# Optimization experiments

Measured on AMD Instinct MI355X. Metric: run time of the kernel, lower is better.

Reference implementation:

```python
import jax, jax.numpy as jnp
import numpy as np

NUM_HEADS = 4
NUM_TOTAL = 100000
N_HEDGE = 32768
N_NODE = 65536
MAX_ARITY_PAD = 10
MAX_VINE = 16
EMBED_DIM = 256
HIDDEN_DIM = 1024
N_LAYERS = 2
K_HOP = 2
POS_VOCAB = 23  # 2*max_arity+3
BATCH_PRED = 256


def setup_inputs() -> dict:
    key = jax.random.key(0)
    ks = jax.random.split(key, 16)
    s = 0.02
    D, FF, L = EMBED_DIM, HIDDEN_DIM, N_LAYERS
    unity_embeddings = jax.random.normal(ks[0], (NUM_TOTAL, D), jnp.float32) * s
    cls_edge_emb = jax.random.normal(ks[1], (1, D), jnp.float32) * s
    pad_edge_emb = jax.random.normal(ks[2], (1, D), jnp.float32) * s
    pos_table = jax.random.normal(ks[3], (POS_VOCAB, D), jnp.float32) * s
    qkv_w = jax.random.normal(ks[4], (L, 3 * D, D), jnp.float32) * s
    qkv_b = jnp.zeros((L, 3 * D), jnp.float32)
    out_w = jax.random.normal(ks[5], (L, D, D), jnp.float32) * s
    out_b = jnp.zeros((L, D), jnp.float32)
    ln1_g = jnp.ones((L, D), jnp.float32); ln1_b = jnp.zeros((L, D), jnp.float32)
    ln2_g = jnp.ones((L, D), jnp.float32); ln2_b = jnp.zeros((L, D), jnp.float32)
    ff1_w = jax.random.normal(ks[6], (L, FF, D), jnp.float32) * s
    ff1_b = jnp.zeros((L, FF), jnp.float32)
    ff2_w = jax.random.normal(ks[7], (L, D, FF), jnp.float32) * s
    ff2_b = jnp.zeros((L, D), jnp.float32)
    # V2E dense batch: entity/rel ids per hyperedge (padded to MAX_ARITY_PAD)
    xid_dense = jax.random.randint(ks[8], (N_HEDGE, MAX_ARITY_PAD), 0, NUM_TOTAL)
    v_mask = jax.random.bernoulli(ks[9], 0.7, (N_HEDGE, MAX_ARITY_PAD)).at[:, 0].set(True)
    x_pos = jax.random.randint(ks[10], (N_HEDGE, MAX_ARITY_PAD), 0, POS_VOCAB - 2)
    x_pos = jnp.where(v_mask, x_pos, POS_VOCAB - 2)  # pad pos id = 2*max_arity+1
    x_pos_dense = jnp.concatenate([jnp.full((N_HEDGE, 1), POS_VOCAB - 1, x_pos.dtype), x_pos], axis=1)  # cls pos id
    # E2V dense batch: hyperedge ids per node; pad id = N_HEDGE, cls id = N_HEDGE+1 (prepended)
    h_mask_body = jax.random.bernoulli(ks[11], 0.6, (N_NODE, MAX_VINE)).at[:, 0].set(True)
    hid_body = jax.random.randint(ks[12], (N_NODE, MAX_VINE), 0, N_HEDGE)
    hid_body = jnp.where(h_mask_body, hid_body, N_HEDGE)
    hid_dense = jnp.concatenate([jnp.full((N_NODE, 1), N_HEDGE + 1, hid_body.dtype), hid_body], axis=1)
    h_mask = jnp.concatenate([jnp.ones((N_NODE, 1), bool), h_mask_body], axis=1)
    subg_ent_id = jax.random.choice(ks[13], NUM_TOTAL, (N_NODE,), replace=False)
    predict_edge_index = jax.random.randint(ks[14], (BATCH_PRED,), 0, N_HEDGE)
    return dict(unity_embeddings=unity_embeddings, cls_edge_emb=cls_edge_emb, pad_edge_emb=pad_edge_emb,
                pos_table=pos_table, qkv_w=qkv_w, qkv_b=qkv_b, out_w=out_w, out_b=out_b,
                ln1_g=ln1_g, ln1_b=ln1_b, ln2_g=ln2_g, ln2_b=ln2_b,
                ff1_w=ff1_w, ff1_b=ff1_b, ff2_w=ff2_w, ff2_b=ff2_b,
                xid_dense=xid_dense, v_mask=v_mask, x_pos_dense=x_pos_dense,
                hid_dense=hid_dense, h_mask=h_mask, subg_ent_id=subg_ent_id,
                predict_edge_index=predict_edge_index, K_hop=K_HOP)


def _ln(x, g, b):
    m = jnp.mean(x, -1, keepdims=True)
    v = jnp.mean((x - m) ** 2, -1, keepdims=True)
    return (x - m) * jax.lax.rsqrt(v + 1e-5) * g + b


def _layer(x, mask, wqkv, bqkv, wo, bo, g1, b1, g2, b2, w1, bb1, w2, bb2):
    # Post-norm torch TransformerEncoderLayer with relu, dropout=0
    B, S, D = x.shape
    H = NUM_HEADS; dh = D // H
    qkv = x @ wqkv.T + bqkv
    q, k, v = jnp.split(qkv, 3, axis=-1)
    heads = lambda t: t.reshape(B, S, H, dh).transpose(0, 2, 1, 3)
    q, k, v = heads(q), heads(k), heads(v)
    scores = jnp.einsum('bhqd,bhkd->bhqk', q, k) / float(np.sqrt(dh))
    scores = jnp.where(mask[:, None, None, :], scores, -1e9)  # key padding mask
    attn = jax.nn.softmax(scores, axis=-1)
    o = jnp.einsum('bhqk,bhkd->bhqd', attn, v).transpose(0, 2, 1, 3).reshape(B, S, D)
    x = _ln(x + o @ wo.T + bo, g1, b1)
    f = jax.nn.relu(x @ w1.T + bb1) @ w2.T + bb2
    return _ln(x + f, g2, b2)


def _encoder(x, mask, qkv_w, qkv_b, out_w, out_b, ln1_g, ln1_b, ln2_g, ln2_b, ff1_w, ff1_b, ff2_w, ff2_b):
    for l in range(qkv_w.shape[0]):
        x = _layer(x, mask, qkv_w[l], qkv_b[l], out_w[l], out_b[l], ln1_g[l], ln1_b[l],
                   ln2_g[l], ln2_b[l], ff1_w[l], ff1_b[l], ff2_w[l], ff2_b[l])
    return x


def reference(unity_embeddings, cls_edge_emb, pad_edge_emb, pos_table, qkv_w, qkv_b, out_w, out_b,
              ln1_g, ln1_b, ln2_g, ln2_b, ff1_w, ff1_b, ff2_w, ff2_b,
              xid_dense, v_mask, x_pos_dense, hid_dense, h_mask, subg_ent_id, predict_edge_index, K_hop):
    D = unity_embeddings.shape[1]
    enc = lambda x, m: _encoder(x, m, qkv_w, qkv_b, out_w, out_b, ln1_g, ln1_b, ln2_g, ln2_b,
                                ff1_w, ff1_b, ff2_w, ff2_b)
    nE = xid_dense.shape[0]
    v_mask_cls = jnp.concatenate([jnp.ones((nE, 1), bool), v_mask], axis=1)
    unity = unity_embeddings
    h_out = None
    for k in range(K_hop + 1):
        # V2E: gather entities per hyperedge, prepend zero CLS, add positions
        xe = unity[xid_dense]                                         # [nE, A, D]
        xe = jnp.concatenate([jnp.zeros((nE, 1, D), xe.dtype), xe], axis=1)
        xe = xe + pos_table[x_pos_dense]
        he = enc(xe, v_mask_cls)[:, 0, :]                             # hedge emb = CLS output
        h_out = he[predict_edge_index]
        if k < K_hop:
            # E2V: hedge table + pad(id=nE) + cls(id=nE+1), gather per node
            ext = jnp.concatenate([he, pad_edge_emb, cls_edge_emb], axis=0)
            ve = ext[hid_dense]                                       # [nN, M+1, D]
            se = enc(ve, h_mask)[:, 0, :]
            unity = unity.at[subg_ent_id].set(se)
    return h_out
```

## Files before the change

### kernel.cpp

```cpp
#include <hip/hip_runtime.h>
#include <stdint.h>

typedef long long i64;
typedef __attribute__((ext_vector_type(8))) short bf16x8;
typedef __attribute__((ext_vector_type(4))) float f32x4;

#define SV 11
#define SE 17
#define ARITY 10
#define NHEDGE 32768
#define NNODE 65536
#define NTOTAL 100000
#define EXTROWS 32896
#define NPRED 256
#define MPRED 2816
#define NN1 2560
#define MN1 43520

__device__ __forceinline__ float b2f(ushort u) {
  union { uint32_t i; float f; } v; v.i = (uint32_t)u << 16; return v.f;
}
__device__ __forceinline__ ushort f2b(float f) {
  union { float f; uint32_t i; } v; v.f = f;
  uint32_t u = v.i + 0x7fffu + ((v.i >> 16) & 1u);
// ... 303 lines not shown
#pragma unroll
    for (int kh = 0; kh < 2; kh++)
#pragma unroll
      for (int m = 0; m < 4; m++)
#pragma unroll
        for (int n = 0; n < 4; n++)
          acc[m][n] = __builtin_amdgcn_mfma_f32_16x16x32_bf16(bf[kh][n], af[kh][m], acc[m][n], 0, 0, 0);
  }

#pragma unroll
  for (int m = 0; m < 4; m++) {
    const int row = m0 + (wr << 6) + (m << 4) + (lane & 15);
#pragma unroll
    for (int n = 0; n < 4; n++) {
      const int col = n0 + (wc << 6) + (n << 4) + ((lane >> 4) << 2);
      float v0 = acc[m][n][0], v1 = acc[m][n][1], v2 = acc[m][n][2], v3 = acc[m][n][3];
      if (MODE > 0) {
        const f32x4 bv = *(const f32x4*)&bias[col];
        v0 += bv[0]; v1 += bv[1]; v2 += bv[2]; v3 += bv[3];
      }
      if (MODE == 2) {
        v0 = fmaxf(v0, 0.f); v1 = fmaxf(v1, 0.f);
        v2 = fmaxf(v2, 0.f); v3 = fmaxf(v3, 0.f);
      }
      uint2 o; o.x = pack2(v0, v1); o.y = pack2(v2, v3);
      *(uint2*)&C[(i64)row * N + col] = o;
    }
  }
}

template <int K>
__global__ __launch_bounds__(512) void gemm_ln_k(const ushort* __restrict__ A,
                                                 const ushort* __restrict__ W,
                                                 const float* __restrict__ bias,
                                                 const ushort* R, int rstride,
                                                 const float* __restrict__ g,
                                                 const float* __restrict__ b,
                                                 ushort* C, int cstride, int M,
                                                 const int* ssn, int nseq,
                                                 const int* rrp) {
  const int m0 = blockIdx.x << 7;
  if (ssn && m0 >= ssn[nseq] - ssn[0]) return;
  __shared__ ushort As[128 * 64];
  __shared__ ushort Ws[256 * 64];
  __shared__ float partS[128][4];
  __shared__ float partQ[128][4];
  const int tid = threadIdx.x;
  const int wave = tid >> 6, lane = tid & 63;
  const int wr = wave >> 2, wc = wave & 3;

  f32x4 acc[4][4];
#pragma unroll
  for (int m = 0; m < 4; m++)
#pragma unroll
    for (int n = 0; n < 4; n++) acc[m][n] = (f32x4){0.f, 0.f, 0.f, 0.f};

  int rowA[2], kgA[2];
#pragma unroll
  for (int i = 0; i < 2; i++) {
    const int u = wave * 128 + i * 64 + lane;
    rowA[i] = u >> 3; kgA[i] = (u & 7) ^ ((u >> 3) & 7);
  }
  int rowW[4], kgW[4];
#pragma unroll
  for (int i = 0; i < 4; i++) {
    const int u = wave * 256 + i * 64 + lane;
    rowW[i] = u >> 3; kgW[i] = (u & 7) ^ ((u >> 3) & 7);
  }

#pragma unroll
  for (int i = 0; i < 2; i++)
    gload_lds16(A + (i64)(m0 + rowA[i]) * K + (kgA[i] << 3),
                (char*)As + (wave * 128 + i * 64) * 16);
#pragma unroll
  for (int i = 0; i < 4; i++)
    gload_lds16(W + (i64)rowW[i] * K + (kgW[i] << 3),
                (char*)Ws + (wave * 256 + i * 64) * 16);

  for (int k0 = 0; k0 < K; k0 += 64) {
    __syncthreads();
    bf16x8 af[2][4], bf[2][4];
#pragma unroll
    for (int kh = 0; kh < 2; kh++) {
      const int kb = (kh << 2) + (lane >> 4);
#pragma unroll
      for (int m = 0; m < 4; m++) {
        const int row = (wr << 6) + (m << 4) + (lane & 15);
        af[kh][m] = *(const bf16x8*)&As[row * 64 + ((kb ^ (row & 7)) << 3)];
      }
#pragma unroll
      for (int n = 0; n < 4; n++) {
        const int row = (wc << 6) + (n << 4) + (lane & 15);
        bf[kh][n] = *(const bf16x8*)&Ws[row * 64 + ((kb ^ (row & 7)) << 3)];
      }
    }
    __syncthreads();
    if (k0 + 64 < K) {
#pragma unroll
      for (int i = 0; i < 2; i++)
        gload_lds16(A + (i64)(m0 + rowA[i]) * K + (k0 + 64) + (kgA[i] << 3),
                    (char*)As + (wave * 128 + i * 64) * 16);
#pragma unroll
      for (int i = 0; i < 4; i++)
        gload_lds16(W + (i64)rowW[i] * K + (k0 + 64) + (kgW[i] << 3),
                    (char*)Ws + (wave * 256 + i * 64) * 16);
    }
#pragma unroll
    for (int kh = 0; kh < 2; kh++)
#pragma unroll
      for (int m = 0; m < 4; m++)
#pragma unroll
        for (int n = 0; n < 4; n++)
          acc[m][n] = __builtin_amdgcn_mfma_f32_16x16x32_bf16(bf[kh][n], af[kh][m], acc[m][n], 0, 0, 0);
  }

#pragma unroll
  for (int m = 0; m < 4; m++) {
    const int tokl = (wr << 6) + (m << 4) + (lane & 15);
    const int row = m0 + tokl;
    const i64 rr = rrp ? (i64)(rrp[row] - rrp[0]) : (i64)row;
    float s = 0.f, q = 0.f;
#pragma unroll
    for (int n = 0; n < 4; n++) {
      const int col = (wc << 6) + (n << 4) + ((lane >> 4) << 2);
      const f32x4 bv = *(const f32x4*)&bias[col];
      const uint2 ru = *(const uint2*)&R[rr * rstride + col];
      float v0 = acc[m][n][0] + bv[0] + b2f((ushort)(ru.x & 0xffff));
      float v1 = acc[m][n][1] + bv[1] + b2f((ushort)(ru.x >> 16));
      float v2 = acc[m][n][2] + bv[2] + b2f((ushort)(ru.y & 0xffff));
      float v3 = acc[m][n][3] + bv[3] + b2f((ushort)(ru.y >> 16));
      acc[m][n][0] = v0; acc[m][n][1] = v1; acc[m][n][2] = v2; acc[m][n][3] = v3;
      s += v0 + v1 + v2 + v3;
      q += v0 * v0 + v1 * v1 + v2 * v2 + v3 * v3;
    }
    s += __shfl_xor(s, 16, 64); s += __shfl_xor(s, 32, 64);
    q += __shfl_xor(q, 16, 64); q += __shfl_xor(q, 32, 64);
    if (lane < 16) { partS[tokl][wc] = s; partQ[tokl][wc] = q; }
  }
  __syncthreads();
#pragma unroll
  for (int m = 0; m < 4; m++) {
    const int tokl = (wr << 6) + (m << 4) + (lane & 15);
    const i64 row = (i64)(m0 + tokl);
    const f32x4 s4 = *(const f32x4*)&partS[tokl][0];
    const f32x4 q4 = *(const f32x4*)&partQ[tokl][0];
    const float mean = (s4[0] + s4[1] + s4[2] + s4[3]) * (1.f / 256.f);
    const float var = (q4[0] + q4[1] + q4[2] + q4[3]) * (1.f / 256.f) - mean * mean;
    const float rs = rsqrtf(var + 1e-5f);
#pragma unroll
    for (int n = 0; n < 4; n++) {
      const int col = (wc << 6) + (n << 4) + ((lane >> 4) << 2);
      const f32x4 g4 = *(const f32x4*)&g[col];
      const f32x4 b4 = *(const f32x4*)&b[col];
      uint2 o;
      o.x = pack2((acc[m][n][0] - mean) * rs * g4[0] + b4[0],
                  (acc[m][n][1] - mean) * rs * g4[1] + b4[1]);
      o.y = pack2((acc[m][n][2] - mean) * rs * g4[2] + b4[2],
                  (acc[m][n][3] - mean) * rs * g4[3] + b4[3]);
      *(uint2*)&C[row * cstride + col] = o;
    }
  }
}

template <int S>
__global__ __launch_bounds__(16 * S) void attn1_k(const ushort* __restrict__ QKV,
                                                  const int* __restrict__ ss,
                                                  ushort* __restrict__ O) {
  __shared__ float KL[4][S][68];
  __shared__ float VL[4][S][68];
  const int tid = threadIdx.x;
  const int s0 = ss[0];
  const int base = ss[blockIdx.x] - s0;
  const int L = ss[blockIdx.x + 1] - ss[blockIdx.x];

  for (int u = tid; u < 128 * L; u += 16 * S) {
    const int d4 = u & 15, h = (u >> 4) & 3, mt = u >> 6;
    const int mat = (mt >= L), t = mat ? mt - L : mt;
    const ushort* gp = QKV + (i64)(base + t) * 768 + 256 + mat * 256 + h * 64 + d4 * 4;
    ushort4 raw = *(const ushort4*)gp;
    float* dst = (mat ? &VL[h][t][0] : &KL[h][t][0]) + d4 * 4;
    dst[0] = b2f(raw.x); dst[1] = b2f(raw.y); dst[2] = b2f(raw.z); dst[3] = b2f(raw.w);
  }
  __syncthreads();

  const int h = tid / (4 * S);
  const int r = tid - h * 4 * S;
  const int q = r >> 2, j = r & 3;
  if (q >= L) return;

  float qv[16];
  {
    const ushort* qp = QKV + (i64)(base + q) * 768 + h * 64 + j * 16;
    cvt8(*(const uint4*)qp, qv);
    cvt8(*(const uint4*)(qp + 8), qv + 8);
  }

  float w[S];
  float mx = -1e30f;
#pragma unroll
  for (int s = 0; s < S; s++) {
    float p = -1e30f;
    if (s < L) {
      const float* kr = &KL[h][s][j * 16];
      p = 0.f;
#pragma unroll
      for (int e = 0; e < 4; e++) {
        const float4 kv = *(const float4*)(kr + e * 4);
        p = fmaf(qv[e * 4 + 0], kv.x, p);
        p = fmaf(qv[e * 4 + 1], kv.y, p);
        p = fmaf(qv[e * 4 + 2], kv.z, p);
        p = fmaf(qv[e * 4 + 3], kv.w, p);
      }
      p += __shfl_xor(p, 1, 64);
      p += __shfl_xor(p, 2, 64);
      p *= 0.125f;
    }
    w[s] = p;
    mx = fmaxf(mx, p);
  }
  float sum = 0.f;
#pragma unroll
  for (int s = 0; s < S; s++) { w[s] = __expf(w[s] - mx); sum += w[s]; }
  const float inv = 1.f / sum;

  float o[16];
#pragma unroll
  for (int e = 0; e < 16; e++) o[e] = 0.f;
#pragma unroll
  for (int s = 0; s < S; s++) {
    if (s < L) {
      const float ws = w[s];
      const float* vr = &VL[h][s][j * 16];
#pragma unroll
      for (int e = 0; e < 4; e++) {
        const float4 vv = *(const float4*)(vr + e * 4);
        o[e * 4 + 0] = fmaf(ws, vv.x, o[e * 4 + 0]);
        o[e * 4 + 1] = fmaf(ws, vv.y, o[e * 4 + 1]);
        o[e * 4 + 2] = fmaf(ws, vv.z, o[e * 4 + 2]);
        o[e * 4 + 3] = fmaf(ws, vv.w, o[e * 4 + 3]);
      }
    }
  }
  uint4 st0, st1;
  st0.x = pack2(o[0] * inv, o[1] * inv);   st0.y = pack2(o[2] * inv, o[3] * inv);
  st0.z = pack2(o[4] * inv, o[5] * inv);   st0.w = pack2(o[6] * inv, o[7] * inv);
  st1.x = pack2(o[8] * inv, o[9] * inv);   st1.y = pack2(o[10] * inv, o[11] * inv);
  st1.z = pack2(o[12] * inv, o[13] * inv); st1.w = pack2(o[14] * inv, o[15] * inv);
  ushort* op = O + (i64)(base + q) * 256 + h * 64 + j * 16;
  *(uint4*)op = st0;
  *(uint4*)(op + 8) = st1;
}

template <int S>
__global__ __launch_bounds__(16 * S) void attn1g_k(const ushort* __restrict__ QKVE,
                                                   const int* __restrict__ gid,
                                                   const int* __restrict__ ss,
                                                   ushort* __restrict__ O) {
  __shared__ float KL[4][S][68];
  __shared__ float VL[4][S][68];
  __shared__ int ids[S];
  const int tid = threadIdx.x;
  const int s0 = ss[0];
  const int base = ss[blockIdx.x] - s0;
  const int L = ss[blockIdx.x + 1] - ss[blockIdx.x];

  if (tid < L) ids[tid] = gid[base + tid];
  __syncthreads();

  for (int u = tid; u < 128 * L; u += 16 * S) {
    const int d4 = u & 15, h = (u >> 4) & 3, mt = u >> 6;
    const int mat = (mt >= L), t = mat ? mt - L : mt;
    const ushort* gp = QKVE + (i64)ids[t] * 768 + 256 + mat * 256 + h * 64 + d4 * 4;
    ushort4 raw = *(const ushort4*)gp;
    float* dst = (mat ? &VL[h][t][0] : &KL[h][t][0]) + d4 * 4;
    dst[0] = b2f(raw.x); dst[1] = b2f(raw.y); dst[2] = b2f(raw.z); dst[3] = b2f(raw.w);
  }
  __syncthreads();

  const int h = tid / (4 * S);
  const int r = tid - h * 4 * S;
  const int q = r >> 2, j = r & 3;
  if (q >= L) return;

  float qv[16];
  {
    const ushort* qp = QKVE + (i64)ids[q] * 768 + h * 64 + j * 16;
    cvt8(*(const uint4*)qp, qv);
    cvt8(*(const uint4*)(qp + 8), qv + 8);
  }

  float w[S];
  float mx = -1e30f;
#pragma unroll
  for (int s = 0; s < S; s++) {
    float p = -1e30f;
    if (s < L) {
      const float* kr = &KL[h][s][j * 16];
      p = 0.f;
#pragma unroll
      for (int e = 0; e < 4; e++) {
        const float4 kv = *(const float4*)(kr + e * 4);
        p = fmaf(qv[e * 4 + 0], kv.x, p);
        p = fmaf(qv[e * 4 + 1], kv.y, p);
        p = fmaf(qv[e * 4 + 2], kv.z, p);
        p = fmaf(qv[e * 4 + 3], kv.w, p);
      }
// ... 224 lines not shown
  const int lane = threadIdx.x & 63;
  ushort4 v = *(const ushort4*)&predHe[(i64)i * 256 + lane * 4];
  float4 o; o.x = b2f(v.x); o.y = b2f(v.y); o.z = b2f(v.z); o.w = b2f(v.w);
  *(float4*)&out[(i64)i * 256 + lane * 4] = o;
}

extern "C" void kernel_launch(void* const* d_in, const int* in_sizes, int n_in,
                              void* d_out, int out_size, void* d_ws, size_t ws_size,
                              hipStream_t stream) {
  (void)in_sizes; (void)n_in; (void)out_size;
  const float* unity_in = (const float*)d_in[0];
  const float* cls_emb  = (const float*)d_in[1];
  const float* pad_emb  = (const float*)d_in[2];
  const float* pos_tab  = (const float*)d_in[3];
  const float* qkv_w    = (const float*)d_in[4];
  const float* qkv_b    = (const float*)d_in[5];
  const float* out_w    = (const float*)d_in[6];
  const float* out_b    = (const float*)d_in[7];
  const float* ln1_g    = (const float*)d_in[8];
  const float* ln1_b    = (const float*)d_in[9];
  const float* ln2_g    = (const float*)d_in[10];
  const float* ln2_b    = (const float*)d_in[11];
  const float* ff1_w    = (const float*)d_in[12];
  const float* ff1_b    = (const float*)d_in[13];
  const float* ff2_w    = (const float*)d_in[14];
  const float* ff2_b    = (const float*)d_in[15];
  const int* xid   = (const int*)d_in[16];
  const int* vmask = (const int*)d_in[17];
  const int* xpos  = (const int*)d_in[18];
  const int* hid   = (const int*)d_in[19];
  const int* hmask = (const int*)d_in[20];
  const int* subg  = (const int*)d_in[21];
  const int* pred  = (const int*)d_in[22];

  const i64 unity_b = (i64)NTOTAL * 256 * 4;
  const i64 ext_b   = (i64)EXTROWS * 256 * 2;
  const i64 qkvE_b  = (i64)EXTROWS * 768 * 2;
  const int nq = 2 * 768 * 256, no = 2 * 256 * 256,
            n1 = 2 * 1024 * 256, n2 = 2 * 256 * 1024;
  const i64 wts_b = (i64)(nq + no + n1 + n2) * 2;
  const i64 idx_b = 16 * 1024 * 1024;
  const i64 per_elem = (i64)SE * (512 + 2048 + 512 + 4);
  int CHUNK = 8192;
  while (CHUNK > 4096 &&
         unity_b + ext_b + qkvE_b + wts_b + idx_b + (i64)CHUNK * per_elem > (i64)ws_size)
    CHUNK >>= 1;
  const int NCH_H = NHEDGE / CHUNK;
  const int NCH_N = NNODE / CHUNK;

  char* w = (char*)d_ws;
  float*  unity = (float*)w;  w += unity_b;
  ushort* ext   = (ushort*)w; w += ext_b;
  ushort* qkvE  = (ushort*)w; w += qkvE_b;
  ushort* wq    = (ushort*)w; w += (i64)nq * 2;
  ushort* wo    = (ushort*)w; w += (i64)no * 2;
  ushort* w1    = (ushort*)w; w += (i64)n1 * 2;
  ushort* w2    = (ushort*)w; w += (i64)n2 * 2;
  ushort* X     = (ushort*)w; w += (i64)CHUNK * SE * 256 * 2;
  ushort* Y     = (ushort*)w; w += (i64)CHUNK * SE * 1024 * 2;
  ushort* O     = (ushort*)w; w += (i64)CHUNK * SE * 256 * 2;
  int* gid    = (int*)w; w += (i64)CHUNK * SE * 4;
  int* inv    = (int*)w; w += (i64)NTOTAL * 4;
  int* cntE   = (int*)w; w += (i64)NNODE * 4;
  int* cntV   = (int*)w; w += (i64)NHEDGE * 4;
  int* partV  = (int*)w; w += 256 * 4;
  int* partN  = (int*)w; w += 256 * 4;
  int* partA  = (int*)w; w += 256 * 4;
  int* partB  = (int*)w; w += 256 * 4;
  int* ssV    = (int*)w; w += (i64)(NHEDGE + 1) * 4;
  int* ssP    = (int*)w; w += 257 * 4;
  int* ssN    = (int*)w; w += (i64)(NN1 + 1) * 4;
  int* nodeL  = (int*)w; w += (i64)NN1 * 4;
  int* cntN   = (int*)w; w += (i64)NN1 * 4;
  int* tokV   = (int*)w; w += (i64)NHEDGE * SV * 4;
  int* tokP   = (int*)w; w += MPRED * 4;
  int* tokN   = (int*)w; w += (i64)MN1 * 4;
  int* gidN   = (int*)w; w += (i64)MN1 * 4;
  int* flagH  = (int*)w; w += (i64)NHEDGE * 4;
  int* flagE  = (int*)w; w += (i64)NTOTAL * 4;
  int* posH   = (int*)w; w += (i64)(NHEDGE + 1) * 4;
  int* posN   = (int*)w; w += (i64)(NNODE + 1) * 4;
  int* hedgeL = (int*)w; w += (i64)NHEDGE * 4;
  int* nodeL0 = (int*)w; w += (i64)NNODE * 4;
  int* cntB   = (int*)w; w += (i64)NHEDGE * 4;
  int* cntC   = (int*)w; w += (i64)NNODE * 4;
  int* cntD   = (int*)w; w += (i64)NNODE * 4;
  int* ssH    = (int*)w; w += (i64)(NHEDGE + 1) * 4;
  int* ssN0   = (int*)w; w += (i64)(NNODE + 1) * 4;
  int* tokH   = (int*)w; w += (i64)NHEDGE * SV * 4;
  int* tokN0  = (int*)w; w += (i64)NNODE * SE * 4;
  int* ssHseq = (int*)w; w += 16 * 4;
  int* ssNseq = (int*)w; w += 16 * 4;
  ushort* predHe = (ushort*)w; w += (i64)NPRED * 256 * 2;
  ushort* Ocls = O;
  ushort* Qcls = O + (i64)CHUNK * 256;
  ushort* X2   = O + (i64)2 * CHUNK * 256;
  ushort* X3   = O + (i64)3 * CHUNK * 256;

  f2b_cvt_k<<<512, 256, 0, stream>>>(qkv_w, wq, nq);
  f2b_cvt_k<<<512, 256, 0, stream>>>(out_w, wo, no);
  f2b_cvt_k<<<512, 256, 0, stream>>>(ff1_w, w1, n1);
  f2b_cvt_k<<<512, 256, 0, stream>>>(ff2_w, w2, n2);
  hipMemcpyAsync(unity, unity_in, unity_b, hipMemcpyDeviceToDevice, stream);
  ext_init_k<<<1, 256, 0, stream>>>(ext, pad_emb, cls_emb);

  cnt_k<<<NHEDGE / 256, 256, 0, stream>>>(vmask, ARITY, 1, cntV, NHEDGE);
  scan1_k<<<NHEDGE / 256, 256, 0, stream>>>(cntV, ssV, partV, NHEDGE);
  scan2_k<<<1, 256, 0, stream>>>(partV, NHEDGE / 256, ssV, NHEDGE);
  scan3_k<<<NHEDGE / 256, 256, 0, stream>>>(ssV, partV, vmask, ARITY, 1, tokV, NHEDGE);
  cnt_k<<<NNODE / 256, 256, 0, stream>>>(hmask, SE, 0, cntE, NNODE);
  predscan_k<<<1, 256, 0, stream>>>(pred, cntV, vmask, ssP, tokP);
  inv_init_k<<<(NTOTAL + 255) / 256, 256, 0, stream>>>(inv, NTOTAL);
  inv_fill_k<<<NNODE / 256, 256, 0, stream>>>(subg, inv, NNODE);
  prednode_k<<<NN1 / 256, 256, 0, stream>>>(pred, xid, vmask, inv, cntE, nodeL, cntN);
  scan1_k<<<NN1 / 256, 256, 0, stream>>>(cntN, ssN, partN, NN1);
  scan2_k<<<1, 256, 0, stream>>>(partN, NN1 / 256, ssN, NN1);
  scan3n_k<<<NN1 / 256, 256, 0, stream>>>(ssN, partN, hmask, nodeL, tokN);
  zero_k<<<NHEDGE / 256, 256, 0, stream>>>(flagH, NHEDGE);
  zero_k<<<(NTOTAL + 255) / 256, 256, 0, stream>>>(flagE, NTOTAL);
  flagH_k<<<(NN1 * SE + 255) / 256, 256, 0, stream>>>(nodeL, hmask, hid, flagH);
  flagE_k<<<NHEDGE * ARITY / 256, 256, 0, stream>>>(flagH, vmask, xid, flagE);
  flagN_k<<<NNODE / 256, 256, 0, stream>>>(flagE, subg, cntC);
  scan1_k<<<NHEDGE / 256, 256, 0, stream>>>(flagH, posH, partA, NHEDGE);
  scan2_k<<<1, 256, 0, stream>>>(partA, NHEDGE / 256, posH, NHEDGE);
  fill_list_k<<<NHEDGE / 256, 256, 0, stream>>>(flagH, posH, partA, hedgeL, NHEDGE);
  cnt_list_k<<<NHEDGE / 256, 256, 0, stream>>>(hedgeL, posH + NHEDGE, cntV, cntB, NHEDGE);
  scan1_k<<<NHEDGE / 256, 256, 0, stream>>>(cntB, ssH, partA, NHEDGE);
  scan2_k<<<1, 256, 0, stream>>>(partA, NHEDGE / 256, ssH, NHEDGE);
  tok_hedge_k<<<NHEDGE / 256, 256, 0, stream>>>(ssH, partA, posH + NHEDGE, hedgeL, vmask, tokH);
  scan1_k<<<NNODE / 256, 256, 0, stream>>>(cntC, posN, partB, NNODE);
  scan2_k<<<1, 256, 0, stream>>>(partB, NNODE / 256, posN, NNODE);
  fill_list_k<<<NNODE / 256, 256, 0, stream>>>(cntC, posN, partB, nodeL0, NNODE);
  cnt_list_k<<<NNODE / 256, 256, 0, stream>>>(nodeL0, posN + NNODE, cntE, cntD, NNODE);
  scan1_k<<<NNODE / 256, 256, 0, stream>>>(cntD, ssN0, partB, NNODE);
  scan2_k<<<1, 256, 0, stream>>>(partB, NNODE / 256, ssN0, NNODE);
  tok_node_k<<<NNODE / 256, 256, 0, stream>>>(ssN0, partB, posN + NNODE, nodeL0, hmask, tokN0);
  seqlim_k<<<1, 64, 0, stream>>>(posH + NHEDGE, CHUNK, NCH_H, ssHseq);
  seqlim_k<<<1, 64, 0, stream>>>(posN + NNODE, CHUNK, NCH_N, ssNseq);

  const i64 KVo = (i64)768 * 256 + (i64)256 * 256;
  const i64 Qo  = (i64)768 * 256;

  for (int c = 0; c < NCH_H; c++) {
    const int e0 = c * CHUNK;
    const int* ssc = ssV + e0;
    const int Mmax = CHUNK * SV;
    gather_v2e_k<<<Mmax / 4, 256, 0, stream>>>(unity, pos_tab, xid, xpos,
                                               tokV, ssc, CHUNK, X);
    gemm_bf16_k<256, 1><<<dim3(6, Mmax / 128), 256, 0, stream>>>(
        X, wq, qkv_b, Y, Mmax, 768, ssc, CHUNK, nullptr);
    attn1_k<SV><<<CHUNK, 16 * SV, 0, stream>>>(Y, ssc, O);
    gemm_ln_k<256><<<Mmax / 128, 512, 0, stream>>>(
        O, wo, out_b, X, 256, ln1_g, ln1_b, X, 256, Mmax, ssc, CHUNK, nullptr);
    gemm_bf16_k<256, 2><<<dim3(8, Mmax / 128), 256, 0, stream>>>(
        X, w1, ff1_b, Y, Mmax, 1024, ssc, CHUNK, nullptr);
    gemm_ln_k<1024><<<Mmax / 128, 512, 0, stream>>>(
        Y, w2, ff2_b, X, 256, ln2_g, ln2_b, X, 256, Mmax, ssc, CHUNK, nullptr);
    gemm_bf16_k<256, 1><<<dim3(4, Mmax / 128), 256, 0, stream>>>(
        X, wq + KVo, qkv_b + 768 + 256, Y, Mmax, 512, ssc, CHUNK, nullptr);
    gemm_bf16_k<256, 1><<<dim3(2, CHUNK / 128), 256, 0, stream>>>(
        X, wq + Qo, qkv_b + 768, Qcls, CHUNK, 256, nullptr, 0, ssc);
    attn_cls_k<SV><<<CHUNK / 16, 256, 0, stream>>>(Qcls, Y, ssc, Ocls);
    gemm_ln_k<256><<<CHUNK / 128, 512, 0, stream>>>(
        Ocls, wo + (i64)256 * 256, out_b + 256, X, 256,
        ln1_g + 256, ln1_b + 256, X2, 256, CHUNK, nullptr, 0, ssc);
    gemm_bf16_k<256, 2><<<dim3(8, CHUNK / 128), 256, 0, stream>>>(
        X2, w1 + (i64)1024 * 256, ff1_b + 1024, Y, CHUNK, 1024, nullptr, 0, nullptr);
    gemm_ln_k<1024><<<CHUNK / 128, 512, 0, stream>>>(
        Y, w2 + (i64)256 * 1024, ff2_b + 256, X2, 256,
        ln2_g + 256, ln2_b + 256, ext + (i64)e0 * 256, 256, CHUNK, nullptr, 0, nullptr);
  }
  gemm_bf16_k<256, 1><<<dim3(6, EXTROWS / 128), 256, 0, stream>>>(
      ext, wq, qkv_b, qkvE, EXTROWS, 768, nullptr, 0, nullptr);

  for (int c = 0; c < NCH_N; c++) {
    const int base = c * CHUNK;
    const int* ssc = ssN0 + base;
    const int* sqc = ssNseq + c;
    const int Mmax = CHUNK * SE;
    gather_e2vc_k<<<Mmax / 4, 256, 0, stream>>>(ext, hid, nodeL0, tokN0, ssc, CHUNK, X, gid);
    attn1g_k<SE><<<CHUNK, 16 * SE, 0, stream>>>(qkvE, gid, ssc, O);
    gemm_ln_k<256><<<Mmax / 128, 512, 0, stream>>>(
        O, wo, out_b, X, 256, ln1_g, ln1_b, X, 256, Mmax, ssc, CHUNK, nullptr);
    gemm_bf16_k<256, 2><<<dim3(8, Mmax / 128), 256, 0, stream>>>(
        X, w1, ff1_b, Y, Mmax, 1024, ssc, CHUNK, nullptr);
    gemm_ln_k<1024><<<Mmax / 128, 512, 0, stream>>>(
        Y, w2, ff2_b, X, 256, ln2_g, ln2_b, X, 256, Mmax, ssc, CHUNK, nullptr);
    gemm_bf16_k<256, 1><<<dim3(4, Mmax / 128), 256, 0, stream>>>(
        X, wq + KVo, qkv_b + 768 + 256, Y, Mmax, 512, ssc, CHUNK, nullptr);
    gemm_bf16_k<256, 1><<<dim3(2, CHUNK / 128), 256, 0, stream>>>(
        X, wq + Qo, qkv_b + 768, Qcls, CHUNK, 256, sqc, 1, ssc);
    attn_cls_k<SE><<<CHUNK / 16, 256, 0, stream>>>(Qcls, Y, ssc, Ocls);
    gemm_ln_k<256><<<CHUNK / 128, 512, 0, stream>>>(
        Ocls, wo + (i64)256 * 256, out_b + 256, X, 256,
        ln1_g + 256, ln1_b + 256, X2, 256, CHUNK, sqc, 1, ssc);
    gemm_bf16_k<256, 2><<<dim3(8, CHUNK / 128), 256, 0, stream>>>(
        X2, w1 + (i64)1024 * 256, ff1_b + 1024, Y, CHUNK, 1024, sqc, 1, nullptr);
    gemm_ln_k<1024><<<CHUNK / 128, 512, 0, stream>>>(
        Y, w2 + (i64)256 * 1024, ff2_b + 256, X2, 256,
        ln2_g + 256, ln2_b + 256, X3, 256, CHUNK, sqc, 1, nullptr);
    scatter_nc_k<<<CHUNK / 4, 256, 0, stream>>>(X3, subg, nodeL0, posN + NNODE,
                                                unity, base);
  }

  for (int c = 0; c < NCH_H; c++) {
    const int base = c * CHUNK;
    const int* ssc = ssH + base;
    const int* sqc = ssHseq + c;
    const int Mmax = CHUNK * SV;
    gather_v2eh_k<<<Mmax / 4, 256, 0, stream>>>(unity, pos_tab, xid, xpos,
                                                hedgeL, tokH, ssc, CHUNK, X);
    gemm_bf16_k<256, 1><<<dim3(6, Mmax / 128), 256, 0, stream>>>(
        X, wq, qkv_b, Y, Mmax, 768, ssc, CHUNK, nullptr);
    attn1_k<SV><<<CHUNK, 16 * SV, 0, stream>>>(Y, ssc, O);
    gemm_ln_k<256><<<Mmax / 128, 512, 0, stream>>>(
        O, wo, out_b, X, 256, ln1_g, ln1_b, X, 256, Mmax, ssc, CHUNK, nullptr);
    gemm_bf16_k<256, 2><<<dim3(8, Mmax / 128), 256, 0, stream>>>(
        X, w1, ff1_b, Y, Mmax, 1024, ssc, CHUNK, nullptr);
    gemm_ln_k<1024><<<Mmax / 128, 512, 0, stream>>>(
        Y, w2, ff2_b, X, 256, ln2_g, ln2_b, X, 256, Mmax, ssc, CHUNK, nullptr);
    gemm_bf16_k<256, 1><<<dim3(4, Mmax / 128), 256, 0, stream>>>(
        X, wq + KVo, qkv_b + 768 + 256, Y, Mmax, 512, ssc, CHUNK, nullptr);
    gemm_bf16_k<256, 1><<<dim3(2, CHUNK / 128), 256, 0, stream>>>(
        X, wq + Qo, qkv_b + 768, Qcls, CHUNK, 256, sqc, 1, ssc);
    attn_cls_k<SV><<<CHUNK / 16, 256, 0, stream>>>(Qcls, Y, ssc, Ocls);
    gemm_ln_k<256><<<CHUNK / 128, 512, 0, stream>>>(
        Ocls, wo + (i64)256 * 256, out_b + 256, X, 256,
        ln1_g + 256, ln1_b + 256, X2, 256, CHUNK, sqc, 1, ssc);
    gemm_bf16_k<256, 2><<<dim3(8, CHUNK / 128), 256, 0, stream>>>(
        X2, w1 + (i64)1024 * 256, ff1_b + 1024, Y, CHUNK, 1024, sqc, 1, nullptr);
    gemm_ln_k<1024><<<CHUNK / 128, 512, 0, stream>>>(
        Y, w2 + (i64)256 * 1024, ff2_b + 256, X2, 256,
        ln2_g + 256, ln2_b + 256, X3, 256, CHUNK, sqc, 1, nullptr);
    scatter_ext_k<<<CHUNK / 4, 256, 0, stream>>>(X3, hedgeL, posH + NHEDGE, ext, base);
  }
  gemm_bf16_k<256, 1><<<dim3(6, EXTROWS / 128), 256, 0, stream>>>(
      ext, wq, qkv_b, qkvE, EXTROWS, 768, nullptr, 0, nullptr);

  {
    gather_e2vc_k<<<MN1 / 4, 256, 0, stream>>>(ext, hid, nodeL, tokN, ssN, NN1, X, gidN);
    attn1g_k<SE><<<NN1, 16 * SE, 0, stream>>>(qkvE, gidN, ssN, O);
    gemm_ln_k<256><<<MN1 / 128, 512, 0, stream>>>(
        O, wo, out_b, X, 256, ln1_g, ln1_b, X, 256, MN1, ssN, NN1, nullptr);
    gemm_bf16_k<256, 2><<<dim3(8, MN1 / 128), 256, 0, stream>>>(
        X, w1, ff1_b, Y, MN1, 1024, ssN, NN1, nullptr);
    gemm_ln_k<1024><<<MN1 / 128, 512, 0, stream>>>(
        Y, w2, ff2_b, X, 256, ln2_g, ln2_b, X, 256, MN1, ssN, NN1, nullptr);
    gemm_bf16_k<256, 1><<<dim3(4, MN1 / 128), 256, 0, stream>>>(
        X, wq + KVo, qkv_b + 768 + 256, Y, MN1, 512, ssN, NN1, nullptr);
    gemm_bf16_k<256, 1><<<dim3(2, NN1 / 128), 256, 0, stream>>>(
        X, wq + Qo, qkv_b + 768, Qcls, NN1, 256, nullptr, 0, ssN);
    attn_cls_k<SE><<<NN1 / 16, 256, 0, stream>>>(Qcls, Y, ssN, Ocls);
    gemm_ln_k<256><<<NN1 / 128, 512, 0, stream>>>(
        Ocls, wo + (i64)256 * 256, out_b + 256, X, 256,
        ln1_g + 256, ln1_b + 256, X2, 256, NN1, nullptr, 0, ssN);
    gemm_bf16_k<256, 2><<<dim3(8, NN1 / 128), 256, 0, stream>>>(
        X2, w1 + (i64)1024 * 256, ff1_b + 1024, Y, NN1, 1024, nullptr, 0, nullptr);
    gemm_ln_k<1024><<<NN1 / 128, 512, 0, stream>>>(
        Y, w2 + (i64)256 * 1024, ff2_b + 256, X2, 256,
        ln2_g + 256, ln2_b + 256, X3, 256, NN1, nullptr, 0, nullptr);
    scatter_nc_k<<<NN1 / 4, 256, 0, stream>>>(X3, subg, nodeL, nullptr, unity, 0);
  }

  {
    const int* ssc = ssP;
    gather_v2e_k<<<MPRED / 4, 256, 0, stream>>>(unity, pos_tab, xid, xpos,
                                                tokP, ssc, NPRED, X);
    gemm_bf16_k<256, 1><<<dim3(6, MPRED / 128), 256, 0, stream>>>(
        X, wq, qkv_b, Y, MPRED, 768, ssc, NPRED, nullptr);
    attn1_k<SV><<<NPRED, 16 * SV, 0, stream>>>(Y, ssc, O);
    gemm_ln_k<256><<<MPRED / 128, 512, 0, stream>>>(
        O, wo, out_b, X, 256, ln1_g, ln1_b, X, 256, MPRED, ssc, NPRED, nullptr);
    gemm_bf16_k<256, 2><<<dim3(8, MPRED / 128), 256, 0, stream>>>(
        X, w1, ff1_b, Y, MPRED, 1024, ssc, NPRED, nullptr);
    gemm_ln_k<1024><<<MPRED / 128, 512, 0, stream>>>(
        Y, w2, ff2_b, X, 256, ln2_g, ln2_b, X, 256, MPRED, ssc, NPRED, nullptr);
    gemm_bf16_k<256, 1><<<dim3(4, MPRED / 128), 256, 0, stream>>>(
        X, wq + KVo, qkv_b + 768 + 256, Y, MPRED, 512, ssc, NPRED, nullptr);
    gemm_bf16_k<256, 1><<<dim3(2, NPRED / 128), 256, 0, stream>>>(
        X, wq + Qo, qkv_b + 768, Qcls, NPRED, 256, nullptr, 0, ssc);
    attn_cls_k<SV><<<NPRED / 16, 256, 0, stream>>>(Qcls, Y, ssc, Ocls);
    gemm_ln_k<256><<<NPRED / 128, 512, 0, stream>>>(
        Ocls, wo + (i64)256 * 256, out_b + 256, X, 256,
        ln1_g + 256, ln1_b + 256, X2, 256, NPRED, nullptr, 0, ssc);
    gemm_bf16_k<256, 2><<<dim3(8, NPRED / 128), 256, 0, stream>>>(
        X2, w1 + (i64)1024 * 256, ff1_b + 1024, Y, NPRED, 1024, nullptr, 0, nullptr);
    gemm_ln_k<1024><<<NPRED / 128, 512, 0, stream>>>(
        Y, w2 + (i64)256 * 1024, ff2_b + 256, X2, 256,
        ln2_g + 256, ln2_b + 256, predHe, 256, NPRED, nullptr, 0, nullptr);
  }
  out_cvt_k<<<NPRED / 4, 256, 0, stream>>>(predHe, (float*)d_out);
}
```

Measured before the change: 7.269 ms.

## Fuse FFN up-projection, ReLU, down-projection and residual LayerNorm into one kernel

Adds an ff_ln_k kernel that, for each tile of 64 rows, computes the 1024-wide hidden activation in 128-column slices. Each slice gets bias and ReLU, is kept in LDS, and is immediately multiplied by the matching slice of W2. Bias, residual add and LayerNorm follow at the end. This replaces the separate FF1 GEMM and FF2+LN GEMM launches in every encoder layer. It is meant to remove the global write and read of the large hidden tensor and halve the launch count. In exchange, the tiles are smaller (64 rows instead of 128), so weight reloads per row go up, and the loop has no double buffering and many barriers.

```diff
diff --git a/kernel.cpp b/kernel.cpp
--- a/kernel.cpp
+++ b/kernel.cpp
@@ -479,6 +479,176 @@
       const int col = (wc << 6) + (n << 4) + ((lane >> 4) << 2);
       const f32x4 g4 = *(const f32x4*)&g[col];
       const f32x4 b4 = *(const f32x4*)&b[col];
+      uint2 o;
+      o.x = pack2((acc[m][n][0] - mean) * rs * g4[0] + b4[0],
+                  (acc[m][n][1] - mean) * rs * g4[1] + b4[1]);
+      o.y = pack2((acc[m][n][2] - mean) * rs * g4[2] + b4[2],
+                  (acc[m][n][3] - mean) * rs * g4[3] + b4[3]);
+      *(uint2*)&C[row * cstride + col] = o;
+    }
+  }
+}
+
+__global__ __launch_bounds__(256) void ff_ln_k(const ushort* __restrict__ A,
+                                               const ushort* __restrict__ W1,
+                                               const float* __restrict__ b1,
+                                               const ushort* __restrict__ W2,
+                                               const float* __restrict__ b2,
+                                               const ushort* R, int rstride,
+                                               const float* __restrict__ g,
+                                               const float* __restrict__ bb,
+                                               ushort* C, int cstride, int M,
+                                               const int* ssn, int nseq) {
+  const int m0 = blockIdx.x << 6;
+  if (ssn && m0 >= ssn[nseq] - ssn[0]) return;
+  __shared__ ushort Ys[64 * 128];
+  __shared__ ushort Stage[256 * 64];
+  __shared__ float partS[64][4];
+  __shared__ float partQ[64][4];
+  const int tid = threadIdx.x;
+  const int wave = tid >> 6, lane = tid & 63;
+
+  f32x4 acc[4][4];
+#pragma unroll
+  for (int m = 0; m < 4; m++)
+#pragma unroll
+    for (int n = 0; n < 4; n++) acc[m][n] = (f32x4){0.f, 0.f, 0.f, 0.f};
+
+  for (int fc = 0; fc < 8; fc++) {
+    f32x4 accY[4][2];
+#pragma unroll
+    for (int m = 0; m < 4; m++)
+#pragma unroll
+      for (int n = 0; n < 2; n++) accY[m][n] = (f32x4){0.f, 0.f, 0.f, 0.f};
+
+    for (int t = 0; t < 4; t++) {
+      const int kk = t << 6;
+#pragma unroll
+      for (int i = 0; i < 2; i++) {
+        const int u = i * 256 + tid;
+        const int row = u >> 3, kg = (u & 7) ^ (row & 7);
+        gload_lds16(A + (i64)(m0 + row) * 256 + kk + (kg << 3), (char*)Stage + u * 16);
+      }
+#pragma unroll
+      for (int i = 0; i < 4; i++) {
+        const int u = i * 256 + tid;
+        const int row = u >> 3, kg = (u & 7) ^ (row & 7);
+        gload_lds16(W1 + (i64)(fc * 128 + row) * 256 + kk + (kg << 3),
+                    (char*)(Stage + 4096) + u * 16);
+      }
+      __syncthreads();
+#pragma unroll
+      for (int kh = 0; kh < 2; kh++) {
+        const int kb = (kh << 2) + (lane >> 4);
+        bf16x8 af[4], bf[2];
+#pragma unroll
+        for (int m = 0; m < 4; m++) {
+          const int row = (m << 4) + (lane & 15);
+          af[m] = *(const bf16x8*)&Stage[row * 64 + ((kb ^ (row & 7)) << 3)];
+        }
+#pragma unroll
+        for (int n = 0; n < 2; n++) {
+          const int row = (wave << 5) + (n << 4) + (lane & 15);
+          bf[n] = *(const bf16x8*)&Stage[4096 + row * 64 + ((kb ^ (row & 7)) << 3)];
+        }
+#pragma unroll
+        for (int m = 0; m < 4; m++)
+#pragma unroll
+          for (int n = 0; n < 2; n++)
+            accY[m][n] = __builtin_amdgcn_mfma_f32_16x16x32_bf16(bf[n], af[m], accY[m][n], 0, 0, 0);
+      }
+      __syncthreads();
+    }
+#pragma unroll
+    for (int m = 0; m < 4; m++) {
+      const int row = (m << 4) + (lane & 15);
+#pragma unroll
+      for (int n = 0; n < 2; n++) {
+        const int colg = (wave << 5) + (n << 4) + ((lane >> 4) << 2);
+        const f32x4 bv = *(const f32x4*)&b1[fc * 128 + colg];
+        const float v0 = fmaxf(accY[m][n][0] + bv[0], 0.f);
+        const float v1 = fmaxf(accY[m][n][1] + bv[1], 0.f);
+        const float v2 = fmaxf(accY[m][n][2] + bv[2], 0.f);
+        const float v3 = fmaxf(accY[m][n][3] + bv[3], 0.f);
+        const int kbY = colg >> 3, off = colg & 7;
+        const int swz = (kbY & 8) | ((kbY ^ (row & 7)) & 7);
+        uint2 o; o.x = pack2(v0, v1); o.y = pack2(v2, v3);
+        *(uint2*)&Ys[row * 128 + swz * 8 + off] = o;
+      }
+    }
+#pragma unroll
+    for (int ks = 0; ks < 2; ks++) {
+#pragma unroll
+      for (int i = 0; i < 8; i++) {
+        const int u = i * 256 + tid;
+        const int row = u >> 3, kg = (u & 7) ^ (row & 7);
+        gload_lds16(W2 + (i64)row * 1024 + fc * 128 + (ks << 6) + (kg << 3),
+                    (char*)Stage + u * 16);
+      }
+      __syncthreads();
+#pragma unroll
+      for (int kh = 0; kh < 2; kh++) {
+        const int kb = (kh << 2) + (lane >> 4);
+        bf16x8 af[4], bf[4];
+#pragma unroll
+        for (int m = 0; m < 4; m++) {
+          const int row = (m << 4) + (lane & 15);
+          const int kbY = (ks << 3) + kb;
+          const int swz = (kbY & 8) | ((kbY ^ (row & 7)) & 7);
+          af[m] = *(const bf16x8*)&Ys[row * 128 + (swz << 3)];
+        }
+#pragma unroll
+        for (int n = 0; n < 4; n++) {
+          const int row = (wave << 6) + (n << 4) + (lane & 15);
+          bf[n] = *(const bf16x8*)&Stage[row * 64 + ((kb ^ (row & 7)) << 3)];
+        }
+#pragma unroll
+        for (int m = 0; m < 4; m++)
+#pragma unroll
+          for (int n = 0; n < 4; n++)
+            acc[m][n] = __builtin_amdgcn_mfma_f32_16x16x32_bf16(bf[n], af[m], acc[m][n], 0, 0, 0);
+      }
+      __syncthreads();
+    }
+  }
+
+#pragma unroll
+  for (int m = 0; m < 4; m++) {
+    const int tokl = (m << 4) + (lane & 15);
+    const i64 row = (i64)(m0 + tokl);
+    float s = 0.f, q = 0.f;
+#pragma unroll
+    for (int n = 0; n < 4; n++) {
+      const int col = (wave << 6) + (n << 4) + ((lane >> 4) << 2);
+      const f32x4 bv = *(const f32x4*)&b2[col];
+      const uint2 ru = *(const uint2*)&R[row * rstride + col];
+      float v0 = acc[m][n][0] + bv[0] + b2f((ushort)(ru.x & 0xffff));
+      float v1 = acc[m][n][1] + bv[1] + b2f((ushort)(ru.x >> 16));
+      float v2 = acc[m][n][2] + bv[2] + b2f((ushort)(ru.y & 0xffff));
+      float v3 = acc[m][n][3] + bv[3] + b2f((ushort)(ru.y >> 16));
+      acc[m][n][0] = v0; acc[m][n][1] = v1; acc[m][n][2] = v2; acc[m][n][3] = v3;
+      s += v0 + v1 + v2 + v3;
+      q += v0 * v0 + v1 * v1 + v2 * v2 + v3 * v3;
+    }
+    s += __shfl_xor(s, 16, 64); s += __shfl_xor(s, 32, 64);
+    q += __shfl_xor(q, 16, 64); q += __shfl_xor(q, 32, 64);
+    if (lane < 16) { partS[tokl][wave] = s; partQ[tokl][wave] = q; }
+  }
+  __syncthreads();
+#pragma unroll
+  for (int m = 0; m < 4; m++) {
+    const int tokl = (m << 4) + (lane & 15);
+    const i64 row = (i64)(m0 + tokl);
+    const f32x4 s4 = *(const f32x4*)&partS[tokl][0];
+    const f32x4 q4 = *(const f32x4*)&partQ[tokl][0];
+    const float mean = (s4[0] + s4[1] + s4[2] + s4[3]) * (1.f / 256.f);
+    const float var = (q4[0] + q4[1] + q4[2] + q4[3]) * (1.f / 256.f) - mean * mean;
+    const float rs = rsqrtf(var + 1e-5f);
+#pragma unroll
+    for (int n = 0; n < 4; n++) {
+      const int col = (wave << 6) + (n << 4) + ((lane >> 4) << 2);
+      const f32x4 g4 = *(const f32x4*)&g[col];
+      const f32x4 b4 = *(const f32x4*)&bb[col];
       uint2 o;
       o.x = pack2((acc[m][n][0] - mean) * rs * g4[0] + b4[0],
                   (acc[m][n][1] - mean) * rs * g4[1] + b4[1]);
@@ -1009,10 +1179,8 @@
     attn1_k<SV><<<CHUNK, 16 * SV, 0, stream>>>(Y, ssc, O);
     gemm_ln_k<256><<<Mmax / 128, 512, 0, stream>>>(
         O, wo, out_b, X, 256, ln1_g, ln1_b, X, 256, Mmax, ssc, CHUNK, nullptr);
-    gemm_bf16_k<256, 2><<<dim3(8, Mmax / 128), 256, 0, stream>>>(
-        X, w1, ff1_b, Y, Mmax, 1024, ssc, CHUNK, nullptr);
-    gemm_ln_k<1024><<<Mmax / 128, 512, 0, stream>>>(
-        Y, w2, ff2_b, X, 256, ln2_g, ln2_b, X, 256, Mmax, ssc, CHUNK, nullptr);
+    ff_ln_k<<<Mmax / 64, 256, 0, stream>>>(
+        X, w1, ff1_b, w2, ff2_b, X, 256, ln2_g, ln2_b, X, 256, Mmax, ssc, CHUNK);
     gemm_bf16_k<256, 1><<<dim3(4, Mmax / 128), 256, 0, stream>>>(
         X, wq + KVo, qkv_b + 768 + 256, Y, Mmax, 512, ssc, CHUNK, nullptr);
     gemm_bf16_k<256, 1><<<dim3(2, CHUNK / 128), 256, 0, stream>>>(
@@ -1021,11 +1189,10 @@
     gemm_ln_k<256><<<CHUNK / 128, 512, 0, stream>>>(
         Ocls, wo + (i64)256 * 256, out_b + 256, X, 256,
         ln1_g + 256, ln1_b + 256, X2, 256, CHUNK, nullptr, 0, ssc);
-    gemm_bf16_k<256, 2><<<dim3(8, CHUNK / 128), 256, 0, stream>>>(
-        X2, w1 + (i64)1024 * 256, ff1_b + 1024, Y, CHUNK, 1024, nullptr, 0, nullptr);
-    gemm_ln_k<1024><<<CHUNK / 128, 512, 0, stream>>>(
-        Y, w2 + (i64)256 * 1024, ff2_b + 256, X2, 256,
-        ln2_g + 256, ln2_b + 256, ext + (i64)e0 * 256, 256, CHUNK, nullptr, 0, nullptr);
+    ff_ln_k<<<CHUNK / 64, 256, 0, stream>>>(
+        X2, w1 + (i64)1024 * 256, ff1_b + 1024, w2 + (i64)256 * 1024, ff2_b + 256,
+        X2, 256, ln2_g + 256, ln2_b + 256, ext + (i64)e0 * 256, 256, CHUNK,
+        nullptr, 0);
   }
   gemm_bf16_k<256, 1><<<dim3(6, EXTROWS / 128), 256, 0, stream>>>(
       ext, wq, qkv_b, qkvE, EXTROWS, 768, nullptr, 0, nullptr);
@@ -1039,10 +1206,8 @@
     attn1g_k<SE><<<CHUNK, 16 * SE, 0, stream>>>(qkvE, gid, ssc, O);
     gemm_ln_k<256><<<Mmax / 128, 512, 0, stream>>>(
         O, wo, out_b, X, 256, ln1_g, ln1_b, X, 256, Mmax, ssc, CHUNK, nullptr);
-    gemm_bf16_k<256, 2><<<dim3(8, Mmax / 128), 256, 0, stream>>>(
-        X, w1, ff1_b, Y, Mmax, 1024, ssc, CHUNK, nullptr);
-    gemm_ln_k<1024><<<Mmax / 128, 512, 0, stream>>>(
-        Y, w2, ff2_b, X, 256, ln2_g, ln2_b, X, 256, Mmax, ssc, CHUNK, nullptr);
+    ff_ln_k<<<Mmax / 64, 256, 0, stream>>>(
+        X, w1, ff1_b, w2, ff2_b, X, 256, ln2_g, ln2_b, X, 256, Mmax, ssc, CHUNK);
     gemm_bf16_k<256, 1><<<dim3(4, Mmax / 128), 256, 0, stream>>>(
         X, wq + KVo, qkv_b + 768 + 256, Y, Mmax, 512, ssc, CHUNK, nullptr);
     gemm_bf16_k<256, 1><<<dim3(2, CHUNK / 128), 256, 0, stream>>>(
@@ -1051,11 +1216,9 @@
     gemm_ln_k<256><<<CHUNK / 128, 512, 0, stream>>>(
         Ocls, wo + (i64)256 * 256, out_b + 256, X, 256,
         ln1_g + 256, ln1_b + 256, X2, 256, CHUNK, sqc, 1, ssc);
-    gemm_bf16_k<256, 2><<<dim3(8, CHUNK / 128), 256, 0, stream>>>(
-        X2, w1 + (i64)1024 * 256, ff1_b + 1024, Y, CHUNK, 1024, sqc, 1, nullptr);
-    gemm_ln_k<1024><<<CHUNK / 128, 512, 0, stream>>>(
-        Y, w2 + (i64)256 * 1024, ff2_b + 256, X2, 256,
-        ln2_g + 256, ln2_b + 256, X3, 256, CHUNK, sqc, 1, nullptr);
+    ff_ln_k<<<CHUNK / 64, 256, 0, stream>>>(
+        X2, w1 + (i64)1024 * 256, ff1_b + 1024, w2 + (i64)256 * 1024, ff2_b + 256,
+        X2, 256, ln2_g + 256, ln2_b + 256, X3, 256, CHUNK, sqc, 1);
     scatter_nc_k<<<CHUNK / 4, 256, 0, stream>>>(X3, subg, nodeL0, posN + NNODE,
                                                 unity, base);
   }
@@ -1072,10 +1235,8 @@
     attn1_k<SV><<<CHUNK, 16 * SV, 0, stream>>>(Y, ssc, O);
     gemm_ln_k<256><<<Mmax / 128, 512, 0, stream>>>(
         O, wo, out_b, X, 256, ln1_g, ln1_b, X, 256, Mmax, ssc, CHUNK, nullptr);
-    gemm_bf16_k<256, 2><<<dim3(8, Mmax / 128), 256, 0, stream>>>(
-        X, w1, ff1_b, Y, Mmax, 1024, ssc, CHUNK, nullptr);
-    gemm_ln_k<1024><<<Mmax / 128, 512, 0, stream>>>(
-        Y, w2, ff2_b, X, 256, ln2_g, ln2_b, X, 256, Mmax, ssc, CHUNK, nullptr);
+    ff_ln_k<<<Mmax / 64, 256, 0, stream>>>(
+        X, w1, ff1_b, w2, ff2_b, X, 256, ln2_g, ln2_b, X, 256, Mmax, ssc, CHUNK);
     gemm_bf16_k<256, 1><<<dim3(4, Mmax / 128), 256, 0, stream>>>(
         X, wq + KVo, qkv_b + 768 + 256, Y, Mmax, 512, ssc, CHUNK, nullptr);
     gemm_bf16_k<256, 1><<<dim3(2, CHUNK / 128), 256, 0, stream>>>(
@@ -1084,11 +1245,9 @@
     gemm_ln_k<256><<<CHUNK / 128, 512, 0, stream>>>(
         Ocls, wo + (i64)256 * 256, out_b + 256, X, 256,
         ln1_g + 256, ln1_b + 256, X2, 256, CHUNK, sqc, 1, ssc);
-    gemm_bf16_k<256, 2><<<dim3(8, CHUNK / 128), 256, 0, stream>>>(
-        X2, w1 + (i64)1024 * 256, ff1_b + 1024, Y, CHUNK, 1024, sqc, 1, nullptr);
-    gemm_ln_k<1024><<<CHUNK / 128, 512, 0, stream>>>(
-        Y, w2 + (i64)256 * 1024, ff2_b + 256, X2, 256,
-        ln2_g + 256, ln2_b + 256, X3, 256, CHUNK, sqc, 1, nullptr);
+    ff_ln_k<<<CHUNK / 64, 256, 0, stream>>>(
+        X2, w1 + (i64)1024 * 256, ff1_b + 1024, w2 + (i64)256 * 1024, ff2_b + 256,
+        X2, 256, ln2_g + 256, ln2_b + 256, X3, 256, CHUNK, sqc, 1);
     scatter_ext_k<<<CHUNK / 4, 256, 0, stream>>>(X3, hedgeL, posH + NHEDGE, ext, base);
   }
   gemm_bf16_k<256, 1><<<dim3(6, EXTROWS / 128), 256, 0, stream>>>(
@@ -1099,10 +1258,8 @@
     attn1g_k<SE><<<NN1, 16 * SE, 0, stream>>>(qkvE, gidN, ssN, O);
     gemm_ln_k<256><<<MN1 / 128, 512, 0, stream>>>(
         O, wo, out_b, X, 256, ln1_g, ln1_b, X, 256, MN1, ssN, NN1, nullptr);
-    gemm_bf16_k<256, 2><<<dim3(8, MN1 / 128), 256, 0, stream>>>(
-        X, w1, ff1_b, Y, MN1, 1024, ssN, NN1, nullptr);
-    gemm_ln_k<1024><<<MN1 / 128, 512, 0, stream>>>(
-        Y, w2, ff2_b, X, 256, ln2_g, ln2_b, X, 256, MN1, ssN, NN1, nullptr);
+    ff_ln_k<<<MN1 / 64, 256, 0, stream>>>(
+        X, w1, ff1_b, w2, ff2_b, X, 256, ln2_g, ln2_b, X, 256, MN1, ssN, NN1);
     gemm_bf16_k<256, 1><<<dim3(4, MN1 / 128), 256, 0, stream>>>(
         X, wq + KVo, qkv_b + 768 + 256, Y, MN1, 512, ssN, NN1, nullptr);
     gemm_bf16_k<256, 1><<<dim3(2, NN1 / 128), 256, 0, stream>>>(
@@ -1111,11 +1268,9 @@
     gemm_ln_k<256><<<NN1 / 128, 512, 0, stream>>>(
         Ocls, wo + (i64)256 * 256, out_b + 256, X, 256,
         ln1_g + 256, ln1_b + 256, X2, 256, NN1, nullptr, 0, ssN);
-    gemm_bf16_k<256, 2><<<dim3(8, NN1 / 128), 256, 0, stream>>>(
-        X2, w1 + (i64)1024 * 256, ff1_b + 1024, Y, NN1, 1024, nullptr, 0, nullptr);
-    gemm_ln_k<1024><<<NN1 / 128, 512, 0, stream>>>(
-        Y, w2 + (i64)256 * 1024, ff2_b + 256, X2, 256,
-        ln2_g + 256, ln2_b + 256, X3, 256, NN1, nullptr, 0, nullptr);
+    ff_ln_k<<<NN1 / 64, 256, 0, stream>>>(
+        X2, w1 + (i64)1024 * 256, ff1_b + 1024, w2 + (i64)256 * 1024, ff2_b + 256,
+        X2, 256, ln2_g + 256, ln2_b + 256, X3, 256, NN1, nullptr, 0);
     scatter_nc_k<<<NN1 / 4, 256, 0, stream>>>(X3, subg, nodeL, nullptr, unity, 0);
   }
 
@@ -1128,10 +1283,8 @@
     attn1_k<SV><<<NPRED, 16 * SV, 0, stream>>>(Y, ssc, O);
     gemm_ln_k<256><<<MPRED / 128, 512, 0, stream>>>(
         O, wo, out_b, X, 256, ln1_g, ln1_b, X, 256, MPRED, ssc, NPRED, nullptr);
-    gemm_bf16_k<256, 2><<<dim3(8, MPRED / 128), 256, 0, stream>>>(
-        X, w1, ff1_b, Y, MPRED, 1024, ssc, NPRED, nullptr);
-    gemm_ln_k<1024><<<MPRED / 128, 512, 0, stream>>>(
-        Y, w2, ff2_b, X, 256, ln2_g, ln2_b, X, 256, MPRED, ssc, NPRED, nullptr);
+    ff_ln_k<<<MPRED / 64, 256, 0, stream>>>(
+        X, w1, ff1_b, w2, ff2_b, X, 256, ln2_g, ln2_b, X, 256, MPRED, ssc, NPRED);
     gemm_bf16_k<256, 1><<<dim3(4, MPRED / 128), 256, 0, stream>>>(
         X, wq + KVo, qkv_b + 768 + 256, Y, MPRED, 512, ssc, NPRED, nullptr);
     gemm_bf16_k<256, 1><<<dim3(2, NPRED / 128), 256, 0, stream>>>(
@@ -1140,11 +1293,9 @@
     gemm_ln_k<256><<<NPRED / 128, 512, 0, stream>>>(
         Ocls, wo + (i64)256 * 256, out_b + 256, X, 256,
         ln1_g + 256, ln1_b + 256, X2, 256, NPRED, nullptr, 0, ssc);
-    gemm_bf16_k<256, 2><<<dim3(8, NPRED / 128), 256, 0, stream>>>(
-        X2, w1 + (i64)1024 * 256, ff1_b + 1024, Y, NPRED, 1024, nullptr, 0, nullptr);
-    gemm_ln_k<1024><<<NPRED / 128, 512, 0, stream>>>(
-        Y, w2 + (i64)256 * 1024, ff2_b + 256, X2, 256,
-        ln2_g + 256, ln2_b + 256, predHe, 256, NPRED, nullptr, 0, nullptr);
+    ff_ln_k<<<NPRED / 64, 256, 0, stream>>>(
+        X2, w1 + (i64)1024 * 256, ff1_b + 1024, w2 + (i64)256 * 1024, ff2_b + 256,
+        X2, 256, ln2_g + 256, ln2_b + 256, predHe, 256, NPRED, nullptr, 0);
   }
   out_cvt_k<<<NPRED / 4, 256, 0, stream>>>(predHe, (float*)d_out);
 }
```

After: 7.087 ms (median of 2 runs). 1.03x faster.
